# Optimization experiments

Measured on AMD Instinct MI355X. Metric: run time of the kernel, lower is better.

Reference implementation:

```python
import jax, jax.numpy as jnp
import numpy as np

EMBED_DIM = 1024
LN_EPS = 1e-5


def _layernorm(x, w, b):
    m = jnp.mean(x, axis=-1, keepdims=True)
    v = jnp.mean(jnp.square(x - m), axis=-1, keepdims=True)
    return (x - m) * jax.lax.rsqrt(v + LN_EPS) * w + b


def _attention(q, k, v, scale):
    # q: [b, sq, d], k/v: [b, sk, d]
    scores = jnp.einsum('bqd,bkd->bqk', q, k) * scale
    probs = jax.nn.softmax(scores, axis=-1)
    return jnp.einsum('bqk,bkd->bqd', probs, v)


def setup_inputs() -> dict:
    key = jax.random.key(0)
    ks = jax.random.split(key, 16)
    B, SQ, SK, D, H = 8, 577, 13271, EMBED_DIM, 4  # H=int(4.0) per source
    return {
        'input_features': jax.random.normal(ks[0], (B, SK, D), jnp.float32),
        'query_feature': jax.random.normal(ks[1], (B, SQ, D), jnp.float32),
        'norm1_w': jax.random.uniform(ks[2], (D,), jnp.float32, 0.5, 1.5),
        'norm1_b': jax.random.normal(ks[3], (D,), jnp.float32) * 0.1,
        'norm2_w': jax.random.uniform(ks[4], (D,), jnp.float32, 0.5, 1.5),
        'norm2_b': jax.random.normal(ks[5], (D,), jnp.float32) * 0.1,
        'norm3_w': jax.random.uniform(ks[6], (D,), jnp.float32, 0.5, 1.5),
        'norm3_b': jax.random.normal(ks[7], (D,), jnp.float32) * 0.1,
        'gamma1': jax.random.uniform(ks[8], (D,), jnp.float32, 0.5, 1.5),
        'gamma2': jax.random.uniform(ks[9], (D,), jnp.float32, 0.5, 1.5),
        'fc1_w': jax.random.normal(ks[10], (H, D), jnp.float32) * (1.0 / np.sqrt(D)),
        'fc1_b': jax.random.normal(ks[11], (H,), jnp.float32) * 0.01,
        'fc2_w': jax.random.normal(ks[12], (D, H), jnp.float32) * (1.0 / np.sqrt(H)),
        'fc2_b': jax.random.normal(ks[13], (D,), jnp.float32) * 0.01,
    }


def reference(input_features, query_feature, norm1_w, norm1_b, norm2_w, norm2_b,
              norm3_w, norm3_b, gamma1, gamma2, fc1_w, fc1_b, fc2_w, fc2_b):
    scale = EMBED_DIM ** (-0.5)
    norm_X = _layernorm(input_features, norm1_w, norm1_b)
    norm_F_L = _layernorm(query_feature, norm2_w, norm2_b)
    # cross attention: query = last-layer feats, key/value = concat of earlier layers
    attended = _attention(norm_F_L, norm_X, norm_X, scale)
    # MLP with exact-erf GELU (torch nn.GELU default), dropout=0 -> identity
    h = jax.nn.gelu(attended @ fc1_w.T + fc1_b, approximate=False)
    cross_attended = h @ fc2_w.T + fc2_b
    norm_cross = _layernorm(cross_attended, norm3_w, norm3_b)
    self_attended = _attention(norm_cross, norm_cross, norm_cross, scale)
    skip_connect = cross_attended + gamma1 * self_attended
    return norm_F_L + gamma2 * skip_connect
```

## Files before the change

### kernel.cpp

```cpp
#include <hip/hip_runtime.h>
#include <hip/hip_bf16.h>
#include <math.h>

typedef unsigned short u16;
typedef __attribute__((ext_vector_type(4))) unsigned short u16x4;
typedef __attribute__((ext_vector_type(8))) __bf16 bf16x8;
typedef __attribute__((ext_vector_type(4))) float fx4;

#define DEV __device__ __forceinline__

DEV u16 f2bf(float f) {
    unsigned u = __float_as_uint(f);
    u += 0x7fffu + ((u >> 16) & 1u);
    return (u16)(u >> 16);
}

DEV void async_load16(const void* g, void* l) {
    __builtin_amdgcn_global_load_lds(
        (const __attribute__((address_space(1))) void*)g,
        (__attribute__((address_space(3))) void*)l, 16, 0, 0);
}

DEV void block_reduce2(float& a, float& b) {
    #pragma unroll
    for (int o = 32; o; o >>= 1) { a += __shfl_xor(a, o); b += __shfl_xor(b, o); }
    __shared__ float sa[4], sb[4];
    const int lane = threadIdx.x & 63, wv = threadIdx.x >> 6;
    if (lane == 0) { sa[wv] = a; sb[wv] = b; }
    __syncthreads();
    a = sa[0] + sa[1] + sa[2] + sa[3];
    b = sb[0] + sb[1] + sb[2] + sb[3];
    __syncthreads();
}

DEV void xcd_swizzle3(int& bx, int& by, int& bz) {
    const int nx = gridDim.x, ny = gridDim.y;
    const int total = nx * ny * gridDim.z;
    const int lin = blockIdx.x + nx * (blockIdx.y + ny * blockIdx.z);
    const int cpx = total >> 3;
    const int swz = (lin & 7) * cpx + (lin >> 3);
    bx = swz % nx;
    const int r = swz / nx;
    by = r % ny;
    bz = r / ny;
}

__global__ __launch_bounds__(256) void ln_k(
    const float* __restrict__ in, int rows_real,
    const float* __restrict__ w, const float* __restrict__ bias,
    u16* __restrict__ out_bf, float* __restrict__ out_f32)
{
    const int r = blockIdx.x, b = blockIdx.y, tid = threadIdx.x;
    const int rows_pad = gridDim.x;
    const size_t orow = ((size_t)b * rows_pad + r) * 1024 + tid * 4;
    if (r >= rows_real) {
        u16x4 z = {0, 0, 0, 0};
        *(u16x4*)&out_bf[orow] = z;
        if (out_f32) { fx4 zf = {0.f, 0.f, 0.f, 0.f}; *(fx4*)&out_f32[orow] = zf; }
        return;
    }
    const size_t irow = ((size_t)b * rows_real + r) * 1024 + tid * 4;
    fx4 x = *(const fx4*)&in[irow];
    float s1 = x.x + x.y + x.z + x.w;
    float s2 = x.x * x.x + x.y * x.y + x.z * x.z + x.w * x.w;
    block_reduce2(s1, s2);
    float m = s1 * (1.0f / 1024.0f);
    float var = s2 * (1.0f / 1024.0f) - m * m;
    float rs = rsqrtf(var + 1e-5f);
    fx4 wv4 = *(const fx4*)&w[tid * 4];
    fx4 bv4 = *(const fx4*)&bias[tid * 4];
    fx4 y;
    y.x = (x.x - m) * rs * wv4.x + bv4.x;
    y.y = (x.y - m) * rs * wv4.y + bv4.y;
    y.z = (x.z - m) * rs * wv4.z + bv4.z;
    y.w = (x.w - m) * rs * wv4.w + bv4.w;
    u16x4 o = { f2bf(y.x), f2bf(y.y), f2bf(y.z), f2bf(y.w) };
    *(u16x4*)&out_bf[orow] = o;
    if (out_f32) *(fx4*)&out_f32[orow] = y;
}

template<bool ATOMIC>
DEV void gemm_body(
    const u16* __restrict__ Ab, const u16* __restrict__ Bb, float* __restrict__ Cb,
    int k_begin, int iters, int lda, int ldb, int ldc)
{
    __shared__ u16 lA[128 * 32];
    __shared__ u16 lB[128 * 32];
    const int lane = threadIdx.x & 63, wv = threadIdx.x >> 6;
    const int wm = (wv >> 1) * 64, wn = (wv & 1) * 64;
    const int frow = lane & 15, quad = lane >> 4;

    fx4 acc[4][4];
    #pragma unroll
    for (int i = 0; i < 4; ++i)
        #pragma unroll
        for (int j = 0; j < 4; ++j) { acc[i][j].x = 0; acc[i][j].y = 0; acc[i][j].z = 0; acc[i][j].w = 0; }

    const int c0 = wv * 64 + lane;
    const int r0a = c0 >> 2, s0 = (c0 & 3) * 8;
    const int c1 = 256 + c0;
    const int r1a = c1 >> 2, s1 = (c1 & 3) * 8;

    for (int it = 0; it < iters; ++it) {
        const int k0 = k_begin + it * 32;
        async_load16(Ab + (size_t)r0a * lda + k0 + s0, &lA[(wv * 64) * 8]);
        async_load16(Ab + (size_t)r1a * lda + k0 + s1, &lA[(256 + wv * 64) * 8]);
        async_load16(Bb + (size_t)r0a * ldb + k0 + s0, &lB[(wv * 64) * 8]);
        async_load16(Bb + (size_t)r1a * ldb + k0 + s1, &lB[(256 + wv * 64) * 8]);
        __syncthreads();
        bf16x8 af[4], bfr[4];
        #pragma unroll
        for (int i = 0; i < 4; ++i) {
            af[i]  = *(const bf16x8*)&lA[(wm + i * 16 + frow) * 32 + quad * 8];
            bfr[i] = *(const bf16x8*)&lB[(wn + i * 16 + frow) * 32 + quad * 8];
        }
        #pragma unroll
        for (int mi = 0; mi < 4; ++mi)
            #pragma unroll
            for (int ni = 0; ni < 4; ++ni)
                acc[mi][ni] = __builtin_amdgcn_mfma_f32_16x16x32_bf16(af[mi], bfr[ni], acc[mi][ni], 0, 0, 0);
        __syncthreads();
    }

    #pragma unroll
    for (int mi = 0; mi < 4; ++mi) {
        #pragma unroll
        for (int r = 0; r < 4; ++r) {
            const int row = wm + mi * 16 + quad * 4 + r;
            #pragma unroll
            for (int ni = 0; ni < 4; ++ni) {
                const int col = wn + ni * 16 + frow;
                if (ATOMIC) atomicAdd(&Cb[(size_t)row * ldc + col], acc[mi][ni][r]);
                else        __builtin_nontemporal_store(acc[mi][ni][r], &Cb[(size_t)row * ldc + col]);
            }
        }
    }
}

__global__ __launch_bounds__(256) void gemm_bt(
    const u16* __restrict__ A, const u16* __restrict__ B, float* __restrict__ C,
    int K, int lda, int ldb, int ldc, long As, long Bs, long Cs)
{
    const int bz = blockIdx.z;
    const u16* Ab = A + (size_t)bz * As + (size_t)blockIdx.y * 128 * lda;
    const u16* Bb = B + (size_t)bz * Bs + (size_t)blockIdx.x * 128 * ldb;
    float* Cb = C + (size_t)bz * Cs + (size_t)blockIdx.y * 128 * ldc + (size_t)blockIdx.x * 128;
    gemm_body<false>(Ab, Bb, Cb, 0, K / 32, lda, ldb, ldc);
}

template<int NS>
__global__ __launch_bounds__(256) void gemm_bt_sk(
    const u16* __restrict__ A, const u16* __restrict__ B, float* __restrict__ C,
    int iters_per, int lda, int ldb, int ldc, long As, long Bs, long Cs)
{
    int bx, by, bzz;
    xcd_swizzle3(bx, by, bzz);
    const int bz = bzz / NS, sp = bzz % NS;
    const u16* Ab = A + (size_t)bz * As + (size_t)by * 128 * lda;
    const u16* Bb = B + (size_t)bz * Bs + (size_t)bx * 128 * ldb;
    float* Cb = C + (size_t)bz * Cs + (size_t)by * 128 * ldc + (size_t)bx * 128;
    gemm_body<true>(Ab, Bb, Cb, sp * iters_per * 32, iters_per, lda, ldb, ldc);
}

template<int EPT4>
__global__ __launch_bounds__(256) void softmax_k(
    const float* __restrict__ S, u16* __restrict__ P,
    int n_real, int n_pad, float scale, long Ss, long Ps)
{
    const int tid = threadIdx.x;
    const float* Sr = S + (size_t)blockIdx.y * Ss + (size_t)blockIdx.x * n_pad;
    u16* Pr = P + (size_t)blockIdx.y * Ps + (size_t)blockIdx.x * n_pad;
    fx4 v[EPT4];
    float mx = -INFINITY;
    #pragma unroll
    for (int i = 0; i < EPT4; ++i) {
        const int base = (i * 256 + tid) * 4;
        fx4 s;
        if (base < n_pad) s = *(const fx4*)&Sr[base];
        else { s.x = -INFINITY; s.y = -INFINITY; s.z = -INFINITY; s.w = -INFINITY; }
        s.x = (base + 0 < n_real) ? s.x * scale : -INFINITY;
        s.y = (base + 1 < n_real) ? s.y * scale : -INFINITY;
        s.z = (base + 2 < n_real) ? s.z * scale : -INFINITY;
        s.w = (base + 3 < n_real) ? s.w * scale : -INFINITY;
        v[i] = s;
        mx = fmaxf(mx, fmaxf(fmaxf(s.x, s.y), fmaxf(s.z, s.w)));
    }
    #pragma unroll
    for (int o = 32; o; o >>= 1) mx = fmaxf(mx, __shfl_xor(mx, o));
    __shared__ float sm[4];
    const int lane = tid & 63, wvi = tid >> 6;
    if (lane == 0) sm[wvi] = mx;
    __syncthreads();
    mx = fmaxf(fmaxf(sm[0], sm[1]), fmaxf(sm[2], sm[3]));
    __syncthreads();
    float sum = 0.f;
    #pragma unroll
    for (int i = 0; i < EPT4; ++i) {
        fx4 e;
        e.x = __expf(v[i].x - mx); e.y = __expf(v[i].y - mx);
        e.z = __expf(v[i].z - mx); e.w = __expf(v[i].w - mx);
        v[i] = e;
        sum += e.x + e.y + e.z + e.w;
    }
    #pragma unroll
    for (int o = 32; o; o >>= 1) sum += __shfl_xor(sum, o);
    if (lane == 0) sm[wvi] = sum;
    __syncthreads();
    sum = sm[0] + sm[1] + sm[2] + sm[3];
    const float inv = 1.0f / sum;
    #pragma unroll
    for (int i = 0; i < EPT4; ++i) {
        const int base = (i * 256 + tid) * 4;
        if (base < n_pad) {
            u16x4 o = { f2bf(v[i].x * inv), f2bf(v[i].y * inv),
                        f2bf(v[i].z * inv), f2bf(v[i].w * inv) };
            *(u16x4*)&Pr[base] = o;
        }
    }
}

__global__ __launch_bounds__(256) void transpose_k(
    const u16* __restrict__ in, u16* __restrict__ out,
    int in_rows, int in_cols, long is, long os)
{
    __shared__ u16 t[64][68];
    const int b = blockIdx.z;
    const u16* I = in + (size_t)b * is;
    u16* O = out + (size_t)b * os;
    const int c0 = blockIdx.x * 64, r0 = blockIdx.y * 64;
    const int cx = threadIdx.x & 15, ry = threadIdx.x >> 4;
    u16x4 a[4];
    #pragma unroll
    for (int k = 0; k < 4; ++k)
        a[k] = *(const u16x4*)&I[(size_t)(r0 + 4 * ry + k) * in_cols + c0 + 4 * cx];
    #pragma unroll
    for (int e = 0; e < 4; ++e) {
        u16x4 o = { a[0][e], a[1][e], a[2][e], a[3][e] };
        *(u16x4*)&t[4 * cx + e][4 * ry] = o;
    }
    __syncthreads();
    #pragma unroll
    for (int k = 0; k < 4; ++k) {
        const int oc = 4 * ry + k;
        *(u16x4*)&O[(size_t)(c0 + oc) * in_rows + r0 + 4 * cx] =
            *(const u16x4*)&t[oc][4 * cx];
    }
}

__global__ __launch_bounds__(256) void mlp_ln_k(
    const float* __restrict__ att, const float* __restrict__ w1, const float* __restrict__ b1,
    const float* __restrict__ w2, const float* __restrict__ b2,
    const float* __restrict__ w3, const float* __restrict__ b3,
    float* __restrict__ ca, u16* __restrict__ nc, int rows_real)
{
    const int q = blockIdx.x, b = blockIdx.y, tid = threadIdx.x;
    const size_t row = ((size_t)b * gridDim.x + q) * 1024 + tid * 4;
    if (q >= rows_real) {
        fx4 zf = {0.f, 0.f, 0.f, 0.f}; u16x4 z = {0, 0, 0, 0};
        *(fx4*)&ca[row] = zf;
        *(u16x4*)&nc[row] = z;
        return;
    }
    fx4 x = *(const fx4*)&att[row];
    float p[4];
    #pragma unroll
    for (int j = 0; j < 4; ++j) {
        fx4 wj = *(const fx4*)&w1[j * 1024 + tid * 4];
        p[j] = x.x * wj.x + x.y * wj.y + x.z * wj.z + x.w * wj.w;
        #pragma unroll
        for (int o = 32; o; o >>= 1) p[j] += __shfl_xor(p[j], o);
    }
    __shared__ float sh[4][4];
    const int lane = tid & 63, wvi = tid >> 6;
    if (lane == 0) { sh[wvi][0] = p[0]; sh[wvi][1] = p[1]; sh[wvi][2] = p[2]; sh[wvi][3] = p[3]; }
    __syncthreads();
    float h[4];
    #pragma unroll
    for (int j = 0; j < 4; ++j) {
        float s = sh[0][j] + sh[1][j] + sh[2][j] + sh[3][j] + b1[j];
        h[j] = 0.5f * s * (1.0f + erff(s * 0.70710678118f));
    }
    float v[4]; float s1 = 0.f, s2 = 0.f;
    #pragma unroll
    for (int e = 0; e < 4; ++e) {
        const int d = tid * 4 + e;
        fx4 wd = *(const fx4*)&w2[d * 4];
        float t = h[0] * wd.x + h[1] * wd.y + h[2] * wd.z + h[3] * wd.w + b2[d];
        v[e] = t; s1 += t; s2 += t * t;
    }
    block_reduce2(s1, s2);
    const float m = s1 * (1.0f / 1024.0f);
    const float var = s2 * (1.0f / 1024.0f) - m * m;
    const float rs = rsqrtf(var + 1e-5f);
    fx4 cav = {v[0], v[1], v[2], v[3]};
    *(fx4*)&ca[row] = cav;
    fx4 w3v = *(const fx4*)&w3[tid * 4], b3v = *(const fx4*)&b3[tid * 4];
    u16x4 o = { f2bf((v[0] - m) * rs * w3v.x + b3v.x), f2bf((v[1] - m) * rs * w3v.y + b3v.y),
                f2bf((v[2] - m) * rs * w3v.z + b3v.z), f2bf((v[3] - m) * rs * w3v.w + b3v.w) };
    *(u16x4*)&nc[row] = o;
}

__global__ __launch_bounds__(256) void final_k(
    const float* __restrict__ nF, const float* __restrict__ ca,
    const float* __restrict__ att2, const float* __restrict__ g1,
    const float* __restrict__ g2, float* __restrict__ out, int sq, int sqp)
{
    const int q = blockIdx.x, b = blockIdx.y, tid = threadIdx.x;
    const size_t wrow = ((size_t)b * sqp + q) * 1024 + tid * 4;
    const size_t orow = ((size_t)b * sq + q) * 1024 + tid * 4;
    fx4 nf = *(const fx4*)&nF[wrow];
    fx4 c  = *(const fx4*)&ca[wrow];
    fx4 a2 = *(const fx4*)&att2[wrow];
    fx4 G1 = *(const fx4*)&g1[tid * 4];
    fx4 G2 = *(const fx4*)&g2[tid * 4];
    fx4 r;
    r.x = nf.x + G2.x * (c.x + G1.x * a2.x);
    r.y = nf.y + G2.y * (c.y + G1.y * a2.y);
    r.z = nf.z + G2.z * (c.z + G1.z * a2.z);
    r.w = nf.w + G2.w * (c.w + G1.w * a2.w);
    *(fx4*)&out[orow] = r;
}

extern "C" void kernel_launch(void* const* d_in, const int* in_sizes, int n_in,
                              void* d_out, int out_size, void* d_ws, size_t ws_size,
                              hipStream_t stream) {
    const float* x_in = (const float*)d_in[0];
    const float* q_in = (const float*)d_in[1];
    const float* n1w = (const float*)d_in[2];
    const float* n1b = (const float*)d_in[3];
    const float* n2w = (const float*)d_in[4];
    const float* n2b = (const float*)d_in[5];
    const float* n3w = (const float*)d_in[6];
    const float* n3b = (const float*)d_in[7];
    const float* g1  = (const float*)d_in[8];
    const float* g2  = (const float*)d_in[9];
    const float* w1  = (const float*)d_in[10];
    const float* b1  = (const float*)d_in[11];
    const float* w2  = (const float*)d_in[12];
    const float* b2  = (const float*)d_in[13];
    float* out = (float*)d_out;

    const int B = 8, SQ = 577, SK = 13271, D = 1024;
    const int SQP = 640, SKP = 13312;
    const float scale = 0.03125f;

    char* ws = (char*)d_ws;
    size_t off = 0;
    auto alloc = [&](size_t n) { size_t o = off; off = (off + n + 255) & ~(size_t)255; return o; };
    u16*   Xn   = (u16*)  (ws + alloc((size_t)B * SKP * D * 2));
    u16*   Xt   = (u16*)  (ws + alloc((size_t)B * D * SKP * 2));
    u16*   Qb   = (u16*)  (ws + alloc((size_t)B * SQP * D * 2));
    float* nF   = (float*)(ws + alloc((size_t)B * SQP * D * 4));
    u16*   P    = (u16*)  (ws + alloc((size_t)B * SQP * SKP * 2));
    float* att  = (float*)(ws + alloc((size_t)B * SQP * D * 4));
    float* CA   = (float*)(ws + alloc((size_t)B * SQP * D * 4));
    u16*   NC   = (u16*)  (ws + alloc((size_t)B * SQP * D * 2));
    u16*   NCt  = (u16*)  (ws + alloc((size_t)B * D * SQP * 2));
    float* S2   = (float*)(ws + alloc((size_t)B * SQP * SQP * 4));
    u16*   P2   = (u16*)  (ws + alloc((size_t)B * SQP * SQP * 2));
    float* att2 = (float*)(ws + alloc((size_t)B * SQP * D * 4));
    const size_t perS1 = (size_t)SQP * SKP * 4;
    size_t room = (ws_size > off) ? (ws_size - off) / perS1 : 1;
    int g = (int)(room < 1 ? 1 : (room > 8 ? 8 : room));
    float* S1 = (float*)(ws + off);
    (void)in_sizes; (void)n_in; (void)out_size;

    ln_k<<<dim3(SKP, B), 256, 0, stream>>>(x_in, SK, n1w, n1b, Xn, nullptr);
    ln_k<<<dim3(SQP, B), 256, 0, stream>>>(q_in, SQ, n2w, n2b, Qb, nF);

    transpose_k<<<dim3(D / 64, SKP / 64, B), 256, 0, stream>>>(
        Xn, Xt, SKP, D, (long)SKP * D, (long)SKP * D);

    for (int b = 0; b < B; b += g) {
        const int nb = (B - b) < g ? (B - b) : g;
        gemm_bt<<<dim3(SKP / 128, SQP / 128, nb), 256, 0, stream>>>(
            Qb + (size_t)b * SQP * D, Xn + (size_t)b * SKP * D, S1,
            D, D, D, SKP, (long)SQP * D, (long)SKP * D, (long)SQP * SKP);
        softmax_k<13><<<dim3(SQP, nb), 256, 0, stream>>>(
            S1, P + (size_t)b * SQP * SKP, SK, SKP, scale,
            (long)SQP * SKP, (long)SQP * SKP);
    }

    hipMemsetAsync(att, 0, (size_t)B * SQP * D * 4, stream);
    gemm_bt_sk<4><<<dim3(D / 128, SQP / 128, B * 4), 256, 0, stream>>>(
        P, Xt, att, 104, SKP, SKP, D,
        (long)SQP * SKP, (long)D * SKP, (long)SQP * D);

    mlp_ln_k<<<dim3(SQP, B), 256, 0, stream>>>(att, w1, b1, w2, b2, n3w, n3b, CA, NC, SQ);

    transpose_k<<<dim3(D / 64, SQP / 64, B), 256, 0, stream>>>(
        NC, NCt, SQP, D, (long)SQP * D, (long)SQP * D);
    hipMemsetAsync(S2, 0, (size_t)B * SQP * SQP * 4, stream);
    gemm_bt_sk<2><<<dim3(SQP / 128, SQP / 128, B * 2), 256, 0, stream>>>(
        NC, NC, S2, 16, D, D, SQP,
        (long)SQP * D, (long)SQP * D, (long)SQP * SQP);
    softmax_k<1><<<dim3(SQP, B), 256, 0, stream>>>(
        S2, P2, SQ, SQP, scale, (long)SQP * SQP, (long)SQP * SQP);
    hipMemsetAsync(att2, 0, (size_t)B * SQP * D * 4, stream);
    gemm_bt_sk<4><<<dim3(D / 128, SQP / 128, B * 4), 256, 0, stream>>>(
        P2, NCt, att2, 5, SQP, SQP, D,
        (long)SQP * SQP, (long)D * SQP, (long)SQP * D);

    final_k<<<dim3(SQ, B), 256, 0, stream>>>(nF, CA, att2, g1, g2, out, SQ, SQP);
}
```

Baseline: 1.375 ms.

## Double-buffer LDS tiles in GEMM body and fold attention scale into query LN

The shared GEMM body now keeps two LDS buffers and issues the async global-to-LDS loads for the next K-slice before running MFMAs on the current one, so load latency can overlap compute. It also multiplies the bf16 query LayerNorm output by the attention scale, letting the first softmax take a scale of 1. The double buffer doubles LDS use per block, which may lower occupancy. The early-issued loads carry no explicit wait on the async transfer before the barrier, so correctness relies on the existing syncthreads. Pre-scaling before bf16 rounding changes rounding slightly.

```diff
diff --git a/kernel.cpp b/kernel.cpp
--- a/kernel.cpp
+++ b/kernel.cpp
@@ -48,7 +48,7 @@
 __global__ __launch_bounds__(256) void ln_k(
     const float* __restrict__ in, int rows_real,
     const float* __restrict__ w, const float* __restrict__ bias,
-    u16* __restrict__ out_bf, float* __restrict__ out_f32)
+    u16* __restrict__ out_bf, float* __restrict__ out_f32, float out_scale)
 {
     const int r = blockIdx.x, b = blockIdx.y, tid = threadIdx.x;
     const int rows_pad = gridDim.x;
@@ -74,7 +74,8 @@
     y.y = (x.y - m) * rs * wv4.y + bv4.y;
     y.z = (x.z - m) * rs * wv4.z + bv4.z;
     y.w = (x.w - m) * rs * wv4.w + bv4.w;
-    u16x4 o = { f2bf(y.x), f2bf(y.y), f2bf(y.z), f2bf(y.w) };
+    u16x4 o = { f2bf(y.x * out_scale), f2bf(y.y * out_scale),
+                f2bf(y.z * out_scale), f2bf(y.w * out_scale) };
     *(u16x4*)&out_bf[orow] = o;
     if (out_f32) *(fx4*)&out_f32[orow] = y;
 }
@@ -84,8 +85,8 @@
     const u16* __restrict__ Ab, const u16* __restrict__ Bb, float* __restrict__ Cb,
     int k_begin, int iters, int lda, int ldb, int ldc)
 {
-    __shared__ u16 lA[128 * 32];
-    __shared__ u16 lB[128 * 32];
+    __shared__ u16 lA[2][128 * 32];
+    __shared__ u16 lB[2][128 * 32];
     const int lane = threadIdx.x & 63, wv = threadIdx.x >> 6;
     const int wm = (wv >> 1) * 64, wn = (wv & 1) * 64;
     const int frow = lane & 15, quad = lane >> 4;
@@ -101,18 +102,24 @@
     const int c1 = 256 + c0;
     const int r1a = c1 >> 2, s1 = (c1 & 3) * 8;
 
+    auto stage = [&](int buf, int it) {
+        const int k0 = k_begin + it * 32;
+        async_load16(Ab + (size_t)r0a * lda + k0 + s0, &lA[buf][(wv * 64) * 8]);
+        async_load16(Ab + (size_t)r1a * lda + k0 + s1, &lA[buf][(256 + wv * 64) * 8]);
+        async_load16(Bb + (size_t)r0a * ldb + k0 + s0, &lB[buf][(wv * 64) * 8]);
+        async_load16(Bb + (size_t)r1a * ldb + k0 + s1, &lB[buf][(256 + wv * 64) * 8]);
+    };
+
+    stage(0, 0);
+    __syncthreads();
+    int cur = 0;
     for (int it = 0; it < iters; ++it) {
-        const int k0 = k_begin + it * 32;
-        async_load16(Ab + (size_t)r0a * lda + k0 + s0, &lA[(wv * 64) * 8]);
-        async_load16(Ab + (size_t)r1a * lda + k0 + s1, &lA[(256 + wv * 64) * 8]);
-        async_load16(Bb + (size_t)r0a * ldb + k0 + s0, &lB[(wv * 64) * 8]);
-        async_load16(Bb + (size_t)r1a * ldb + k0 + s1, &lB[(256 + wv * 64) * 8]);
-        __syncthreads();
+        if (it + 1 < iters) stage(cur ^ 1, it + 1);
         bf16x8 af[4], bfr[4];
         #pragma unroll
         for (int i = 0; i < 4; ++i) {
-            af[i]  = *(const bf16x8*)&lA[(wm + i * 16 + frow) * 32 + quad * 8];
-            bfr[i] = *(const bf16x8*)&lB[(wn + i * 16 + frow) * 32 + quad * 8];
+            af[i]  = *(const bf16x8*)&lA[cur][(wm + i * 16 + frow) * 32 + quad * 8];
+            bfr[i] = *(const bf16x8*)&lB[cur][(wn + i * 16 + frow) * 32 + quad * 8];
         }
         #pragma unroll
         for (int mi = 0; mi < 4; ++mi)
@@ -120,6 +127,7 @@
             for (int ni = 0; ni < 4; ++ni)
                 acc[mi][ni] = __builtin_amdgcn_mfma_f32_16x16x32_bf16(af[mi], bfr[ni], acc[mi][ni], 0, 0, 0);
         __syncthreads();
+        cur ^= 1;
     }
 
     #pragma unroll
@@ -365,8 +373,8 @@
     float* S1 = (float*)(ws + off);
     (void)in_sizes; (void)n_in; (void)out_size;
 
-    ln_k<<<dim3(SKP, B), 256, 0, stream>>>(x_in, SK, n1w, n1b, Xn, nullptr);
-    ln_k<<<dim3(SQP, B), 256, 0, stream>>>(q_in, SQ, n2w, n2b, Qb, nF);
+    ln_k<<<dim3(SKP, B), 256, 0, stream>>>(x_in, SK, n1w, n1b, Xn, nullptr, 1.0f);
+    ln_k<<<dim3(SQP, B), 256, 0, stream>>>(q_in, SQ, n2w, n2b, Qb, nF, scale);
 
     transpose_k<<<dim3(D / 64, SKP / 64, B), 256, 0, stream>>>(
         Xn, Xt, SKP, D, (long)SKP * D, (long)SKP * D);
@@ -377,7 +385,7 @@
             Qb + (size_t)b * SQP * D, Xn + (size_t)b * SKP * D, S1,
             D, D, D, SKP, (long)SQP * D, (long)SKP * D, (long)SQP * SKP);
         softmax_k<13><<<dim3(SQP, nb), 256, 0, stream>>>(
-            S1, P + (size_t)b * SQP * SKP, SK, SKP, scale,
+            S1, P + (size_t)b * SQP * SKP, SK, SKP, 1.0f,
             (long)SQP * SKP, (long)SQP * SKP);
     }
 
```

Result: faster. 1.347 ms (-2.0%).
